# Performance work log

Measured on AMD Instinct MI355X. Metric: run time of the kernel, lower is better.

Reference implementation:

```python
import jax, jax.numpy as jnp
import numpy as np

N_NODES = 100000
N_EDGES = 1600000
D_IN = 64
D_HID = 64
NEG_SLOPE = 0.01  # torch.nn.LeakyReLU default


def gcn_conv(x, W, b, src, dst, n_nodes):
    h = x @ W  # [N, F_out]
    deg = jnp.zeros((n_nodes,), x.dtype).at[dst].add(jnp.ones((src.shape[0],), x.dtype)) + 1.0
    dinv_sqrt = jax.lax.rsqrt(deg)
    norm = dinv_sqrt[src] * dinv_sqrt[dst]  # [E]
    agg = jnp.zeros_like(h).at[dst].add(norm[:, None] * h[src])
    agg = agg + h * (1.0 / deg)[:, None]  # self-loop contribution: deg^-1/2_i * deg^-1/2_i
    return agg + b


def leaky_relu(v):
    return jnp.where(v >= 0, v, NEG_SLOPE * v)


def setup_inputs() -> dict:
    key = jax.random.key(0)
    ks = jax.random.split(key, 8)
    x = jax.random.normal(ks[0], (N_NODES, D_IN), dtype=jnp.float32)
    edge_index = jax.random.randint(ks[1], (2, N_EDGES), 0, N_NODES, dtype=jnp.int32)
    s = 0.05
    W1 = jax.random.normal(ks[2], (D_IN, D_HID), dtype=jnp.float32) * s
    b1 = jnp.zeros((D_HID,), jnp.float32)
    W2 = jax.random.normal(ks[3], (D_HID, D_HID), dtype=jnp.float32) * s
    b2 = jnp.zeros((D_HID,), jnp.float32)
    W3 = jax.random.normal(ks[4], (D_HID, D_HID), dtype=jnp.float32) * s
    b3 = jnp.zeros((D_HID,), jnp.float32)
    return {"x": x, "W1": W1, "b1": b1, "W2": W2, "b2": b2, "W3": W3, "b3": b3,
            "edge_index": edge_index}


def reference(x, W1, b1, W2, b2, W3, b3, edge_index):
    src, dst = edge_index[0], edge_index[1]
    n = x.shape[0]
    # layer 1: conv -> LeakyReLU -> dropout (identity in eval / reference)
    h = leaky_relu(gcn_conv(x, W1, b1, src, dst, n))
    # layer 2: checkpoint(conv2, ...) -> plain conv, no activation
    h = gcn_conv(h, W2, b2, src, dst, n)
    # layer 3: conv -> LeakyReLU
    h = leaky_relu(gcn_conv(h, W3, b3, src, dst, n))
    return h
```

## Files before the change

kernel.cpp:

```cpp
#include <hip/hip_runtime.h>
#include <hip/hip_fp16.h>
#include <math.h>


constexpr int SHIFT = 8;
constexpr int CHUNK = 4096;
constexpr int BCAP  = 5120;

typedef _Float16 half8 __attribute__((ext_vector_type(8)));
typedef float floatx4 __attribute__((ext_vector_type(4)));

__device__ inline int scan256(int v, int tid, int* wsum, int* total) {
    int lane = tid & 63, w = tid >> 6;
    int inc = v;
#pragma unroll
    for (int off = 1; off < 64; off <<= 1) {
        int t = __shfl_up(inc, off);
        if (lane >= off) inc += t;
    }
    if (lane == 63) wsum[w] = inc;
    __syncthreads();
    int s0 = wsum[0], s1 = wsum[1], s2 = wsum[2], s3 = wsum[3];
    __syncthreads();
    int base = (w > 0 ? s0 : 0) + (w > 1 ? s1 : 0) + (w > 2 ? s2 : 0);
    *total = s0 + s1 + s2 + s3;
    return base + (inc - v);
}

__global__ void k_hist(const int* __restrict__ dst, int E, int NB,
                       int* __restrict__ Bh, int* __restrict__ Bc) {
    __shared__ int h[512];
    int tid = threadIdx.x;
    for (int i = tid; i < 512; i += 256) h[i] = 0;
    __syncthreads();
    int s = blockIdx.x * CHUNK;
    int e = min(s + CHUNK, E);
    for (int i = s + tid; i < e; i += 256) atomicAdd(&h[dst[i] >> SHIFT], 1);
    __syncthreads();
    for (int i = tid; i < NB; i += 256) {
        int v = h[i];
        Bh[(size_t)blockIdx.x * NB + i] = v;
        Bc[(size_t)blockIdx.x * NB + i] = v;
    }
}

__global__ void k_bucket_scan(int* __restrict__ Bh, int B1, int NB,
                              int* __restrict__ total) {
    __shared__ int wsum[4];
    int b = blockIdx.x;
    int tid = threadIdx.x;
    int carry = 0;
    for (int j0 = 0; j0 < B1; j0 += 256) {
        int j = j0 + tid;
        int v = (j < B1) ? Bh[(size_t)j * NB + b] : 0;
        int tot;
        int ex = scan256(v, tid, wsum, &tot);
        if (j < B1) Bh[(size_t)j * NB + b] = ex + carry;
        carry += tot;
    }
    if (tid == 0) total[b] = carry;
}

__global__ void k_base_scan(const int* __restrict__ total, int NB, int E,
                            int* __restrict__ base) {
    __shared__ int wsum[4];
    int tid = threadIdx.x;
    int b0 = 2 * tid, b1 = 2 * tid + 1;
    int v0 = (b0 < NB) ? total[b0] : 0;
    int v1 = (b1 < NB) ? total[b1] : 0;
    int tot;
    int ex = scan256(v0 + v1, tid, wsum, &tot);
    if (b0 < NB) base[b0] = ex;
    if (b1 < NB) base[b1] = ex + v0;
    if (tid == 0) base[NB] = E;
}

__global__ void k_scatter(const int* __restrict__ src, const int* __restrict__ dst,
                          int E, int NB, const int* __restrict__ Bh,
                          const int* __restrict__ Bc, const int* __restrict__ base,
                          unsigned* __restrict__ ebuf) {
    __shared__ int cur[512];
    __shared__ int gb[512];
    __shared__ int wsum[4];
    __shared__ unsigned srec[CHUNK];
    __shared__ int spos[CHUNK];
    int tid = threadIdx.x;
    int j = blockIdx.x;

    int b0 = 2 * tid, b1 = 2 * tid + 1;
    int c0 = (b0 < NB) ? Bc[(size_t)j * NB + b0] : 0;
    int c1 = (b1 < NB) ? Bc[(size_t)j * NB + b1] : 0;
    int tot;
    int ex = scan256(c0 + c1, tid, wsum, &tot);
    if (b0 < NB) {
        cur[b0] = ex;
        gb[b0]  = base[b0] + Bh[(size_t)j * NB + b0] - ex;
    }
    if (b1 < NB) {
        int ex1 = ex + c0;
        cur[b1] = ex1;
        gb[b1]  = base[b1] + Bh[(size_t)j * NB + b1] - ex1;
    }
    __syncthreads();

    int s = j * CHUNK;
    int e = min(s + CHUNK, E);
    for (int i = s + tid; i < e; i += 256) {
        int d = dst[i];
        int b = d >> SHIFT;
        unsigned rec = ((unsigned)(d & 255) << 24) | (unsigned)src[i];
        int lpos = atomicAdd(&cur[b], 1);
        srec[lpos] = rec;
        spos[lpos] = gb[b] + lpos;
    }
    __syncthreads();
    int cntE = e - s;
    for (int t = tid; t < cntE; t += 256) ebuf[spos[t]] = srec[t];
}

__global__ void k_bucket_sort(const unsigned* __restrict__ ebuf,
                              const int* __restrict__ base, int n, int E,
                              int* __restrict__ row_ptr, int* __restrict__ col) {
    __shared__ int cnt[256];
    __shared__ int cur[256];
    __shared__ int wsum[4];
    __shared__ unsigned raw[BCAP];
    __shared__ int sorted[BCAP];
    int b = blockIdx.x;
    int tid = threadIdx.x;
    int s = base[b];
    int e = base[b + 1];
    int len = e - s;
    cnt[tid] = 0;
    __syncthreads();
    if (len <= BCAP) {
        for (int t = tid; t < len; t += 256) {
            unsigned v = ebuf[s + t];
            raw[t] = v;
            atomicAdd(&cnt[v >> 24], 1);
        }
        __syncthreads();
        int tot;
        int ex = scan256(cnt[tid], tid, wsum, &tot);
        int node = (b << SHIFT) | tid;
        if (node < n) row_ptr[node] = s + ex;
        cur[tid] = ex;
        __syncthreads();
        for (int t = tid; t < len; t += 256) {
            unsigned v = raw[t];
            int lpos = atomicAdd(&cur[v >> 24], 1);
            sorted[lpos] = (int)((v & 0x00FFFFFFu) << 7);
        }
        __syncthreads();
        for (int t = tid; t < len; t += 256) col[s + t] = sorted[t];
    } else {
        for (int i = s + tid; i < e; i += 256) atomicAdd(&cnt[ebuf[i] >> 24], 1);
        __syncthreads();
        int tot;
        int ex = scan256(cnt[tid], tid, wsum, &tot);
        int node = (b << SHIFT) | tid;
        if (node < n) row_ptr[node] = s + ex;
        cur[tid] = ex;
        __syncthreads();
        for (int i = s + tid; i < e; i += 256) {
            unsigned v = ebuf[i];
            int lpos = atomicAdd(&cur[v >> 24], 1);
            col[s + lpos] = (int)((v & 0x00FFFFFFu) << 7);
        }
    }
    if (b == 0 && tid == 0) row_ptr[n] = E;
}

__device__ inline void load_bfrag(const float* __restrict__ W, int tid,
                                  half8* b1, half8* b2) {
    int lane = tid & 63;
    int colg = (tid >> 6) * 16 + (lane & 15);
    int k0 = (lane >> 4) * 8;
    half8 x1, x2;
#pragma unroll
    for (int j = 0; j < 8; j++) {
        x1[j] = (_Float16)W[(k0 + j) * 64 + colg];
        x2[j] = (_Float16)W[(k0 + 32 + j) * 64 + colg];
    }
    *b1 = x1;
    *b2 = x2;
}

__device__ inline void mfma_rows_store(const _Float16* rowS, const float* dinvS,
                                       half8 b1, half8 b2, int n, int blockRow0,
                                       int tid, __half* __restrict__ HSn) {
    int w = tid >> 6;
    int lane = tid & 63;
    int ar = lane & 15;
    int ks = lane >> 4;

    half8 a1 = *(const half8*)&rowS[ar * 72 + ks * 8];
    half8 a2 = *(const half8*)&rowS[ar * 72 + 32 + ks * 8];

    floatx4 acc = {0.f, 0.f, 0.f, 0.f};
    acc = __builtin_amdgcn_mfma_f32_16x16x32_f16(a1, b1, acc, 0, 0, 0);
    acc = __builtin_amdgcn_mfma_f32_16x16x32_f16(a2, b2, acc, 0, 0, 0);

    int node0 = (lane >> 4) * 4;
    float4 dv4 = *(const float4*)&dinvS[node0];
    int colg = w * 16 + (lane & 15);
    int base_node = blockRow0 + node0;
#pragma unroll
    for (int reg = 0; reg < 4; reg++) {
        int node_g = base_node + reg;
        if (node_g < n) {
            float dv = (reg == 0) ? dv4.x : (reg == 1) ? dv4.y : (reg == 2) ? dv4.z : dv4.w;
            HSn[(size_t)node_g * 64 + colg] = __float2half(acc[reg] * dv);
        }
    }
}

__global__ void k_gemm_scale(const float* __restrict__ X, const float* __restrict__ W,
                             const int* __restrict__ row_ptr, int n,
                             __half* __restrict__ HS) {
    __shared__ _Float16 rowS[16 * 72];
    __shared__ float dinvS[16];
    int tid = threadIdx.x;

    half8 b1, b2;
    load_bfrag(W, tid, &b1, &b2);

    int g = tid >> 4;
    int c = tid & 15;
    int gid = blockIdx.x * 16 + g;
    if (gid < n) {
        float4 xv = *(const float4*)&X[(size_t)gid * 64 + c * 4];
        __half2 h0 = __floats2half2_rn(xv.x, xv.y);
        __half2 h1 = __floats2half2_rn(xv.z, xv.w);
        uint2 pack;
        pack.x = *(const unsigned int*)&h0;
        pack.y = *(const unsigned int*)&h1;
        *(uint2*)&rowS[g * 72 + c * 4] = pack;
        if (c == 0)
            dinvS[g] = rsqrtf(1.0f + (float)(row_ptr[gid + 1] - row_ptr[gid]));
    }
    __syncthreads();
    mfma_rows_store(rowS, dinvS, b1, b2, n, blockIdx.x * 16, tid, HS);
}

__device__ inline float4 cvt_h4(uint2 v) {
    float2 f0 = __half22float2(*(__half2*)&v.x);
    float2 f1 = __half22float2(*(__half2*)&v.y);
    return make_float4(f0.x, f0.y, f1.x, f1.y);
}

__device__ inline uint2 ld_row(const char* HSb, int boff, int c) {
    return *(const uint2*)(HSb + boff + (c << 3));
}

__device__ inline float4 agg_row(const char* __restrict__ HSb,
                                 const int* __restrict__ col,
                                 int gid, int c, int r0, int r1) {
    float4 a0 = cvt_h4(*(const uint2*)(HSb + ((size_t)gid << 7) + (c << 3)));
    float4 a1 = make_float4(0.f, 0.f, 0.f, 0.f);
    float4 a2 = a1, a3 = a1;
    int e = r0;
    for (; e + 8 <= r1; e += 8) {
        int s0 = col[e + 0], s1 = col[e + 1], s2 = col[e + 2], s3 = col[e + 3];
        int s4 = col[e + 4], s5 = col[e + 5], s6 = col[e + 6], s7 = col[e + 7];
        uint2 v0 = ld_row(HSb, s0, c), v1 = ld_row(HSb, s1, c);
        uint2 v2 = ld_row(HSb, s2, c), v3 = ld_row(HSb, s3, c);
        uint2 v4 = ld_row(HSb, s4, c), v5 = ld_row(HSb, s5, c);
        uint2 v6 = ld_row(HSb, s6, c), v7 = ld_row(HSb, s7, c);
        float4 f0 = cvt_h4(v0), f1 = cvt_h4(v1), f2 = cvt_h4(v2), f3 = cvt_h4(v3);
        float4 f4 = cvt_h4(v4), f5 = cvt_h4(v5), f6 = cvt_h4(v6), f7 = cvt_h4(v7);
        a0.x += f0.x; a0.y += f0.y; a0.z += f0.z; a0.w += f0.w;
        a1.x += f1.x; a1.y += f1.y; a1.z += f1.z; a1.w += f1.w;
        a2.x += f2.x; a2.y += f2.y; a2.z += f2.z; a2.w += f2.w;
        a3.x += f3.x; a3.y += f3.y; a3.z += f3.z; a3.w += f3.w;
        a0.x += f4.x; a0.y += f4.y; a0.z += f4.z; a0.w += f4.w;
        a1.x += f5.x; a1.y += f5.y; a1.z += f5.z; a1.w += f5.w;
        a2.x += f6.x; a2.y += f6.y; a2.z += f6.z; a2.w += f6.w;
        a3.x += f7.x; a3.y += f7.y; a3.z += f7.z; a3.w += f7.w;
    }
    if (e + 4 <= r1) {
        int s0 = col[e + 0], s1 = col[e + 1], s2 = col[e + 2], s3 = col[e + 3];
        uint2 v0 = ld_row(HSb, s0, c), v1 = ld_row(HSb, s1, c);
        uint2 v2 = ld_row(HSb, s2, c), v3 = ld_row(HSb, s3, c);
        float4 f0 = cvt_h4(v0), f1 = cvt_h4(v1), f2 = cvt_h4(v2), f3 = cvt_h4(v3);
        a0.x += f0.x; a0.y += f0.y; a0.z += f0.z; a0.w += f0.w;
        a1.x += f1.x; a1.y += f1.y; a1.z += f1.z; a1.w += f1.w;
        a2.x += f2.x; a2.y += f2.y; a2.z += f2.z; a2.w += f2.w;
        a3.x += f3.x; a3.y += f3.y; a3.z += f3.z; a3.w += f3.w;
        e += 4;
    }
    if (e + 0 < r1) {
        float4 f = cvt_h4(ld_row(HSb, col[e + 0], c));
        a0.x += f.x; a0.y += f.y; a0.z += f.z; a0.w += f.w;
    }
    if (e + 1 < r1) {
        float4 f = cvt_h4(ld_row(HSb, col[e + 1], c));
        a1.x += f.x; a1.y += f.y; a1.z += f.z; a1.w += f.w;
    }
    if (e + 2 < r1) {
        float4 f = cvt_h4(ld_row(HSb, col[e + 2], c));
        a2.x += f.x; a2.y += f.y; a2.z += f.z; a2.w += f.w;
    }
    float4 s;
    s.x = (a0.x + a1.x) + (a2.x + a3.x);
    s.y = (a0.y + a1.y) + (a2.y + a3.y);
    s.z = (a0.z + a1.z) + (a2.z + a3.z);
    s.w = (a0.w + a1.w) + (a2.w + a3.w);
    return s;
}

template <bool RELU>
__global__ void k_agg_gemm(const __half* __restrict__ HS, const int* __restrict__ row_ptr,
                           const int* __restrict__ col, const float* __restrict__ bias,
                           const float* __restrict__ Wn, int n,
                           __half* __restrict__ HSn) {
    __shared__ _Float16 rowS[16 * 72];
    __shared__ float dinvS[16];
    int tid = threadIdx.x;

    half8 b1, b2;
    load_bfrag(Wn, tid, &b1, &b2);

    int g = tid >> 4;
    int c = tid & 15;
    int gid = blockIdx.x * 16 + g;

    if (gid < n) {
        const char* __restrict__ HSb = (const char*)HS;
        int r0 = row_ptr[gid];
        int r1 = row_ptr[gid + 1];
        float4 s = agg_row(HSb, col, gid, c, r0, r1);
        float deg = 1.0f + (float)(r1 - r0);
        float dinv = rsqrtf(deg);
        float4 bv = *(const float4*)&bias[4 * c];
        float vx = dinv * s.x + bv.x;
        float vy = dinv * s.y + bv.y;
        float vz = dinv * s.z + bv.z;
        float vw = dinv * s.w + bv.w;
        if (RELU) {
            vx = (vx >= 0.f) ? vx : 0.01f * vx;
            vy = (vy >= 0.f) ? vy : 0.01f * vy;
            vz = (vz >= 0.f) ? vz : 0.01f * vz;
            vw = (vw >= 0.f) ? vw : 0.01f * vw;
        }
        __half2 h0 = __floats2half2_rn(vx, vy);
        __half2 h1 = __floats2half2_rn(vz, vw);
        uint2 pack;
        pack.x = *(const unsigned int*)&h0;
        pack.y = *(const unsigned int*)&h1;
        *(uint2*)&rowS[g * 72 + c * 4] = pack;
        if (c == 0) dinvS[g] = dinv;
    }
    __syncthreads();
    mfma_rows_store(rowS, dinvS, b1, b2, n, blockIdx.x * 16, tid, HSn);
}

__global__ void k_agg_out(const __half* __restrict__ HS, const int* __restrict__ row_ptr,
                          const int* __restrict__ col, const float* __restrict__ bias,
                          int n, float* __restrict__ out) {
    int gid = (int)((blockIdx.x * (unsigned)blockDim.x + threadIdx.x) >> 4);
    if (gid >= n) return;
    int c = threadIdx.x & 15;
    const char* __restrict__ HSb = (const char*)HS;
    int r0 = row_ptr[gid];
    int r1 = row_ptr[gid + 1];
    float4 s = agg_row(HSb, col, gid, c, r0, r1);
    float deg = 1.0f + (float)(r1 - r0);
    float dinv = rsqrtf(deg);
    float4 bv = *(const float4*)&bias[4 * c];
    float vx = dinv * s.x + bv.x;
    float vy = dinv * s.y + bv.y;
    float vz = dinv * s.z + bv.z;
    float vw = dinv * s.w + bv.w;
    vx = (vx >= 0.f) ? vx : 0.01f * vx;
    vy = (vy >= 0.f) ? vy : 0.01f * vy;
    vz = (vz >= 0.f) ? vz : 0.01f * vz;
    vw = (vw >= 0.f) ? vw : 0.01f * vw;
    *(float4*)&out[(size_t)gid * 64 + 4 * c] = make_float4(vx, vy, vz, vw);
}

static inline size_t align256(size_t x) { return (x + 255) & ~(size_t)255; }

extern "C" void kernel_launch(void* const* d_in, const int* in_sizes, int n_in,
                              void* d_out, int out_size, void* d_ws, size_t ws_size,
                              hipStream_t stream) {
    const float* x  = (const float*)d_in[0];
    const float* W1 = (const float*)d_in[1];
    const float* b1 = (const float*)d_in[2];
    const float* W2 = (const float*)d_in[3];
    const float* b2 = (const float*)d_in[4];
    const float* W3 = (const float*)d_in[5];
    const float* b3 = (const float*)d_in[6];
    const int* edge = (const int*)d_in[7];

    int n = in_sizes[0] / 64;
    int E = in_sizes[7] / 2;
    const int* srcp = edge;
    const int* dstp = edge + E;

    int NB = (n + 255) >> SHIFT;
    int B1 = (E + CHUNK - 1) / CHUNK;

    char* ws = (char*)d_ws;
    int* row_ptr   = (int*)ws;      ws += align256((size_t)(n + 1) * 4);
    int* Bh        = (int*)ws;      ws += align256((size_t)B1 * NB * 4);
    int* Bc        = (int*)ws;      ws += align256((size_t)B1 * NB * 4);
    int* total     = (int*)ws;      ws += align256((size_t)NB * 4);
    int* base      = (int*)ws;      ws += align256((size_t)(NB + 1) * 4);
    unsigned* ebuf = (unsigned*)ws; ws += align256((size_t)E * 4);
    int* col       = (int*)ws;      ws += align256((size_t)E * 4);
    __half* hs_a   = (__half*)ws;   ws += align256((size_t)n * 64 * 2);
    __half* hs_b   = (__half*)ws;   ws += align256((size_t)n * 64 * 2);
    float* out     = (float*)d_out;

    k_hist<<<B1, 256, 0, stream>>>(dstp, E, NB, Bh, Bc);
    k_bucket_scan<<<NB, 256, 0, stream>>>(Bh, B1, NB, total);
    k_base_scan<<<1, 256, 0, stream>>>(total, NB, E, base);
    k_scatter<<<B1, 256, 0, stream>>>(srcp, dstp, E, NB, Bh, Bc, base, ebuf);
    k_bucket_sort<<<NB, 256, 0, stream>>>(ebuf, base, n, E, row_ptr, col);

    int blocks16 = (n + 15) / 16;

    k_gemm_scale<<<blocks16, 256, 0, stream>>>(x, W1, row_ptr, n, hs_a);
    k_agg_gemm<true><<<blocks16, 256, 0, stream>>>(hs_a, row_ptr, col, b1, W2, n, hs_b);
    k_agg_gemm<false><<<blocks16, 256, 0, stream>>>(hs_b, row_ptr, col, b2, W3, n, hs_a);
    k_agg_out<<<blocks16, 256, 0, stream>>>(hs_a, row_ptr, col, b3, n, out);
}
```

Measured before the change: 158.4 us.

## Fold base scan into scatter/sort and pre-transpose weights to fp16

Removes the single-block k_base_scan launch. Each k_scatter and k_bucket_sort block now recomputes the prefix sum of bucket totals itself. Adds a small k_prep kernel that converts W1..W3 to transposed fp16, so each GEMM block loads its B fragments as two 16-byte vector loads instead of 16 strided float loads with conversion. This trades one launch and strided weight reads for redundant per-block scans and one extra tiny launch.

```diff
diff --git a/kernel.cpp b/kernel.cpp
--- a/kernel.cpp
+++ b/kernel.cpp
@@ -25,6 +25,21 @@
     int base = (w > 0 ? s0 : 0) + (w > 1 ? s1 : 0) + (w > 2 ? s2 : 0);
     *total = s0 + s1 + s2 + s3;
     return base + (inc - v);
+}
+
+__global__ void k_prep(const float* __restrict__ W1, const float* __restrict__ W2,
+                       const float* __restrict__ W3, _Float16* __restrict__ Wt) {
+    int tid = threadIdx.x;
+    const float* Ws[3] = {W1, W2, W3};
+    const float* W = Ws[blockIdx.x];
+    _Float16* dst = Wt + (size_t)blockIdx.x * 4096;
+#pragma unroll
+    for (int j = 0; j < 16; j++) {
+        int idx = tid + 256 * j;
+        float v = W[idx];
+        int k = idx >> 6, c = idx & 63;
+        dst[c * 64 + k] = (_Float16)v;
+    }
 }
 
 __global__ void k_hist(const int* __restrict__ dst, int E, int NB,
@@ -61,23 +76,9 @@
     if (tid == 0) total[b] = carry;
 }
 
-__global__ void k_base_scan(const int* __restrict__ total, int NB, int E,
-                            int* __restrict__ base) {
-    __shared__ int wsum[4];
-    int tid = threadIdx.x;
-    int b0 = 2 * tid, b1 = 2 * tid + 1;
-    int v0 = (b0 < NB) ? total[b0] : 0;
-    int v1 = (b1 < NB) ? total[b1] : 0;
-    int tot;
-    int ex = scan256(v0 + v1, tid, wsum, &tot);
-    if (b0 < NB) base[b0] = ex;
-    if (b1 < NB) base[b1] = ex + v0;
-    if (tid == 0) base[NB] = E;
-}
-
 __global__ void k_scatter(const int* __restrict__ src, const int* __restrict__ dst,
                           int E, int NB, const int* __restrict__ Bh,
-                          const int* __restrict__ Bc, const int* __restrict__ base,
+                          const int* __restrict__ Bc, const int* __restrict__ total,
                           unsigned* __restrict__ ebuf) {
     __shared__ int cur[512];
     __shared__ int gb[512];
@@ -88,18 +89,22 @@
     int j = blockIdx.x;
 
     int b0 = 2 * tid, b1 = 2 * tid + 1;
+    int t0 = (b0 < NB) ? total[b0] : 0;
+    int t1 = (b1 < NB) ? total[b1] : 0;
+    int tot;
+    int exb = scan256(t0 + t1, tid, wsum, &tot);
+    int base0 = exb, base1 = exb + t0;
     int c0 = (b0 < NB) ? Bc[(size_t)j * NB + b0] : 0;
     int c1 = (b1 < NB) ? Bc[(size_t)j * NB + b1] : 0;
-    int tot;
     int ex = scan256(c0 + c1, tid, wsum, &tot);
     if (b0 < NB) {
         cur[b0] = ex;
-        gb[b0]  = base[b0] + Bh[(size_t)j * NB + b0] - ex;
+        gb[b0]  = base0 + Bh[(size_t)j * NB + b0] - ex;
     }
     if (b1 < NB) {
         int ex1 = ex + c0;
         cur[b1] = ex1;
-        gb[b1]  = base[b1] + Bh[(size_t)j * NB + b1] - ex1;
+        gb[b1]  = base1 + Bh[(size_t)j * NB + b1] - ex1;
     }
     __syncthreads();
 
@@ -119,20 +124,28 @@
 }
 
 __global__ void k_bucket_sort(const unsigned* __restrict__ ebuf,
-                              const int* __restrict__ base, int n, int E,
+                              const int* __restrict__ total, int n, int E, int NB,
                               int* __restrict__ row_ptr, int* __restrict__ col) {
     __shared__ int cnt[256];
     __shared__ int cur[256];
+    __shared__ int pre[512];
     __shared__ int wsum[4];
     __shared__ unsigned raw[BCAP];
     __shared__ int sorted[BCAP];
     int b = blockIdx.x;
     int tid = threadIdx.x;
-    int s = base[b];
-    int e = base[b + 1];
-    int len = e - s;
+    int v0 = (tid < NB) ? total[tid] : 0;
+    int v1 = (tid + 256 < NB) ? total[tid + 256] : 0;
+    int tot0, tot1;
+    int ex0 = scan256(v0, tid, wsum, &tot0);
+    int ex1 = scan256(v1, tid, wsum, &tot1);
+    pre[tid] = ex0;
+    pre[tid + 256] = tot0 + ex1;
     cnt[tid] = 0;
     __syncthreads();
+    int s = pre[b];
+    int len = total[b];
+    int e = s + len;
     if (len <= BCAP) {
         for (int t = tid; t < len; t += 256) {
             unsigned v = ebuf[s + t];
@@ -171,19 +184,14 @@
     if (b == 0 && tid == 0) row_ptr[n] = E;
 }
 
-__device__ inline void load_bfrag(const float* __restrict__ W, int tid,
+__device__ inline void load_bfrag(const _Float16* __restrict__ Wt, int tid,
                                   half8* b1, half8* b2) {
     int lane = tid & 63;
     int colg = (tid >> 6) * 16 + (lane & 15);
     int k0 = (lane >> 4) * 8;
-    half8 x1, x2;
-#pragma unroll
-    for (int j = 0; j < 8; j++) {
-        x1[j] = (_Float16)W[(k0 + j) * 64 + colg];
-        x2[j] = (_Float16)W[(k0 + 32 + j) * 64 + colg];
-    }
-    *b1 = x1;
-    *b2 = x2;
+    const half8* Wt8 = (const half8*)(Wt + colg * 64 + k0);
+    *b1 = Wt8[0];
+    *b2 = Wt8[4];
 }
 
 __device__ inline void mfma_rows_store(const _Float16* rowS, const float* dinvS,
@@ -215,7 +223,7 @@
     }
 }
 
-__global__ void k_gemm_scale(const float* __restrict__ X, const float* __restrict__ W,
+__global__ void k_gemm_scale(const float* __restrict__ X, const _Float16* __restrict__ Wt,
                              const int* __restrict__ row_ptr, int n,
                              __half* __restrict__ HS) {
     __shared__ _Float16 rowS[16 * 72];
@@ -223,7 +231,7 @@
     int tid = threadIdx.x;
 
     half8 b1, b2;
-    load_bfrag(W, tid, &b1, &b2);
+    load_bfrag(Wt, tid, &b1, &b2);
 
     int g = tid >> 4;
     int c = tid & 15;
@@ -312,14 +320,14 @@
 template <bool RELU>
 __global__ void k_agg_gemm(const __half* __restrict__ HS, const int* __restrict__ row_ptr,
                            const int* __restrict__ col, const float* __restrict__ bias,
-                           const float* __restrict__ Wn, int n,
+                           const _Float16* __restrict__ Wt, int n,
                            __half* __restrict__ HSn) {
     __shared__ _Float16 rowS[16 * 72];
     __shared__ float dinvS[16];
     int tid = threadIdx.x;
 
     half8 b1, b2;
-    load_bfrag(Wn, tid, &b1, &b2);
+    load_bfrag(Wt, tid, &b1, &b2);
 
     int g = tid >> 4;
     int c = tid & 15;
@@ -402,27 +410,27 @@
     int B1 = (E + CHUNK - 1) / CHUNK;
 
     char* ws = (char*)d_ws;
-    int* row_ptr   = (int*)ws;      ws += align256((size_t)(n + 1) * 4);
-    int* Bh        = (int*)ws;      ws += align256((size_t)B1 * NB * 4);
-    int* Bc        = (int*)ws;      ws += align256((size_t)B1 * NB * 4);
-    int* total     = (int*)ws;      ws += align256((size_t)NB * 4);
-    int* base      = (int*)ws;      ws += align256((size_t)(NB + 1) * 4);
-    unsigned* ebuf = (unsigned*)ws; ws += align256((size_t)E * 4);
-    int* col       = (int*)ws;      ws += align256((size_t)E * 4);
-    __half* hs_a   = (__half*)ws;   ws += align256((size_t)n * 64 * 2);
-    __half* hs_b   = (__half*)ws;   ws += align256((size_t)n * 64 * 2);
+    int* row_ptr   = (int*)ws;        ws += align256((size_t)(n + 1) * 4);
+    int* Bh        = (int*)ws;        ws += align256((size_t)B1 * NB * 4);
+    int* Bc        = (int*)ws;        ws += align256((size_t)B1 * NB * 4);
+    int* total     = (int*)ws;        ws += align256((size_t)NB * 4);
+    _Float16* Wt   = (_Float16*)ws;   ws += align256((size_t)3 * 4096 * 2);
+    unsigned* ebuf = (unsigned*)ws;   ws += align256((size_t)E * 4);
+    int* col       = (int*)ws;        ws += align256((size_t)E * 4);
+    __half* hs_a   = (__half*)ws;     ws += align256((size_t)n * 64 * 2);
+    __half* hs_b   = (__half*)ws;     ws += align256((size_t)n * 64 * 2);
     float* out     = (float*)d_out;
 
+    k_prep<<<3, 256, 0, stream>>>(W1, W2, W3, Wt);
     k_hist<<<B1, 256, 0, stream>>>(dstp, E, NB, Bh, Bc);
     k_bucket_scan<<<NB, 256, 0, stream>>>(Bh, B1, NB, total);
-    k_base_scan<<<1, 256, 0, stream>>>(total, NB, E, base);
-    k_scatter<<<B1, 256, 0, stream>>>(srcp, dstp, E, NB, Bh, Bc, base, ebuf);
-    k_bucket_sort<<<NB, 256, 0, stream>>>(ebuf, base, n, E, row_ptr, col);
+    k_scatter<<<B1, 256, 0, stream>>>(srcp, dstp, E, NB, Bh, Bc, total, ebuf);
+    k_bucket_sort<<<NB, 256, 0, stream>>>(ebuf, total, n, E, NB, row_ptr, col);
 
     int blocks16 = (n + 15) / 16;
 
-    k_gemm_scale<<<blocks16, 256, 0, stream>>>(x, W1, row_ptr, n, hs_a);
-    k_agg_gemm<true><<<blocks16, 256, 0, stream>>>(hs_a, row_ptr, col, b1, W2, n, hs_b);
-    k_agg_gemm<false><<<blocks16, 256, 0, stream>>>(hs_b, row_ptr, col, b2, W3, n, hs_a);
+    k_gemm_scale<<<blocks16, 256, 0, stream>>>(x, Wt, row_ptr, n, hs_a);
+    k_agg_gemm<true><<<blocks16, 256, 0, stream>>>(hs_a, row_ptr, col, b1, Wt + 4096, n, hs_b);
+    k_agg_gemm<false><<<blocks16, 256, 0, stream>>>(hs_b, row_ptr, col, b2, Wt + 8192, n, hs_a);
     k_agg_out<<<blocks16, 256, 0, stream>>>(hs_a, row_ptr, col, b3, n, out);
 }
```

New measurement: 162.3 us. +2.4%, slower.
